# Optimization experiments

Hardware: AMD Instinct MI355X
Metric: run time of the kernel (lower is better)

The kernel has to match this reference:

```python
import jax, jax.numpy as jnp
import numpy as np

V = 25000
E = 100000
NODE_IN = 74
EDGE_IN = 12
OUT = 64
EHID = 128
NUM_STEPS = 6


def setup_inputs() -> dict:
    key = jax.random.key(0)
    ks = jax.random.split(key, 12)
    s = 0.05
    node_feats = jax.random.normal(ks[0], (V, NODE_IN), dtype=jnp.float32)
    edge_feats = jax.random.normal(ks[1], (E, EDGE_IN), dtype=jnp.float32)
    src = jax.random.randint(ks[2], (E,), 0, V)
    dst = jax.random.randint(ks[3], (E,), 0, V)
    # project_node_feats: Linear(node_in, out)
    Wp = jax.random.normal(ks[4], (NODE_IN, OUT), dtype=jnp.float32) * s
    bp = jnp.zeros((OUT,), dtype=jnp.float32)
    # edge network: Linear(edge_in, ehid) -> ReLU -> Linear(ehid, out*out)
    We1 = jax.random.normal(ks[5], (EDGE_IN, EHID), dtype=jnp.float32) * s
    be1 = jnp.zeros((EHID,), dtype=jnp.float32)
    We2 = jax.random.normal(ks[6], (EHID, OUT * OUT), dtype=jnp.float32) * s
    be2 = jnp.zeros((OUT * OUT,), dtype=jnp.float32)
    # NNConv output bias
    bias = jnp.zeros((OUT,), dtype=jnp.float32)
    return {
        "node_feats": node_feats, "edge_feats": edge_feats,
        "src": src, "dst": dst,
        "Wp": Wp, "bp": bp,
        "We1": We1, "be1": be1, "We2": We2, "be2": be2,
        "bias": bias,
    }


def reference(node_feats, edge_feats, src, dst, Wp, bp, We1, be1, We2, be2, bias):
    # project node features
    h = jax.nn.relu(node_feats @ Wp + bp)  # [V, OUT]
    # per-edge weight matrices (same every step -> hoist out of loop)
    ew = jax.nn.relu(edge_feats @ We1 + be1) @ We2 + be2  # [E, OUT*OUT]
    ew = ew.reshape(E, OUT, OUT)
    for _ in range(NUM_STEPS):
        # gather src node feats, batched matvec, scatter-sum to dst
        msg = jnp.einsum('ei,eio->eo', h[src], ew)  # [E, OUT]
        agg = jax.ops.segment_sum(msg, dst, num_segments=V)  # [V, OUT]
        h = jax.nn.relu(agg + bias)
    return h
```

## Files before the change

kernel.cpp:

```cpp
#include <hip/hip_runtime.h>
#include <hip/hip_bf16.h>

#define Vn 25000
#define En 100000
#define NODE_IN 74
#define EDGE_IN 12
#define OUTD 64
#define EHID 128
#define NUM_STEPS 6

typedef __attribute__((ext_vector_type(8))) _Float16 half8;
typedef __attribute__((ext_vector_type(4))) float floatx4;

__global__ void proj_kernel(const float* __restrict__ node,
                            const float* __restrict__ Wp,
                            const float* __restrict__ bp,
                            float* __restrict__ h) {
  __shared__ float nf[NODE_IN];
  int v = blockIdx.x;
  int o = threadIdx.x;
  for (int i = o; i < NODE_IN; i += 64) nf[i] = node[(size_t)v * NODE_IN + i];
  __syncthreads();
  float acc = bp[o];
  for (int i = 0; i < NODE_IN; ++i) acc = fmaf(nf[i], Wp[i * OUTD + o], acc);
  h[(size_t)v * OUTD + o] = fmaxf(acc, 0.0f);
}

__global__ void edge_kernel(const float* __restrict__ ef,
                            const float* __restrict__ We1,
                            const float* __restrict__ be1,
                            _Float16* __restrict__ f) {
  __shared__ float es[EDGE_IN];
  int e = blockIdx.x;
  int k = threadIdx.x;
  if (k < EDGE_IN) es[k] = ef[(size_t)e * EDGE_IN + k];
  __syncthreads();
  float acc = be1[k];
  for (int j = 0; j < EDGE_IN; ++j) acc = fmaf(es[j], We1[j * EHID + k], acc);
  f[(size_t)e * EHID + k] = (_Float16)fmaxf(acc, 0.0f);
}

__global__ void w2r_kernel(const float* __restrict__ We2,
                           _Float16* __restrict__ w2s) {
  int g = blockIdx.x * 256 + threadIdx.x;
  int j = g & 7;
  int quad = (g >> 3) & 3;
  int l15 = (g >> 5) & 15;
  int c = (g >> 9) & 3;
  int step = g >> 11;
  int s = step & 3;
  int i = step >> 2;
  int k = s * 32 + quad * 8 + j;
  int col = i * 64 + c * 16 + l15;
  int eidx = g & 2047;
  int estore = eidx ^ (((eidx >> 6) & 3) << 3);
  w2s[((size_t)step << 11) | estore] = (_Float16)We2[(size_t)k * (OUTD * OUTD) + col];
}

#define GLOAD_LDS(gp, lp)                                                     \
  __builtin_amdgcn_global_load_lds(                                           \
      (const __attribute__((address_space(1))) void*)(gp),                    \
      (__attribute__((address_space(3))) void*)(lp), 16, 0, 0)

__global__ __launch_bounds__(64, 2) void msg_kernel(
    const float* __restrict__ h,
    const _Float16* __restrict__ f,
    const _Float16* __restrict__ w2s,
    const int* __restrict__ src,
    const int* __restrict__ dst,
    const float* __restrict__ be2,
    float* __restrict__ agg) {
  __shared__ __align__(16) char smem_raw[16384];
  __shared__ int s_dst[64];

  _Float16* h16 = (_Float16*)smem_raw;
  char* ring = smem_raw + 8192;

  const int lane = threadIdx.x;
  const int quad = lane >> 4;
  const int l15 = lane & 15;
  const int e0 = blockIdx.x * 64;

  {
    int eg = e0 + lane;
    s_dst[lane] = (eg < En) ? dst[eg] : -1;
    int sv = (eg < En) ? src[eg] : 0;
    const float4* hp = reinterpret_cast<const float4*>(h + (size_t)sv * OUTD);
#pragma unroll
    for (int c = 0; c < 16; ++c) {
      float4 v = hp[c];
      h16[(c * 4 + 0) * 64 + lane] = (_Float16)v.x;
      h16[(c * 4 + 1) * 64 + lane] = (_Float16)v.y;
      h16[(c * 4 + 2) * 64 + lane] = (_Float16)v.z;
      h16[(c * 4 + 3) * 64 + lane] = (_Float16)v.w;
    }
  }

  half8 afr[4][4];
#pragma unroll
  for (int t = 0; t < 4; ++t) {
    int e = e0 + t * 16 + l15;
    if (e >= En) e = En - 1;
    const _Float16* fr = f + (size_t)e * EHID + quad * 8;
#pragma unroll
    for (int s = 0; s < 4; ++s)
      afr[t][s] = *reinterpret_cast<const half8*>(fr + s * 32);
  }

  floatx4 acc[4][4];
  const floatx4 zero4 = (floatx4){0.f, 0.f, 0.f, 0.f};
#pragma unroll
  for (int t = 0; t < 4; ++t)
#pragma unroll
    for (int c = 0; c < 4; ++c) acc[t][c] = zero4;

  const char* w2b = (const char*)w2s;
  const int roff = l15 * 64 + ((quad ^ ((l15 >> 1) & 3)) << 4);
  const char* sp0 = ring + roff;
  const char* sp1 = ring + 4096 + roff;

#define STAGE(GS, SLOT)                                                       \
  {                                                                           \
    const char* gp_ = w2b + (size_t)(GS) * 4096 + lane * 16;                  \
    char* lp_ = ring + (SLOT) * 4096;                                         \
    GLOAD_LDS(gp_, lp_);                                                      \
    GLOAD_LDS(gp_ + 1024, lp_ + 1024);                                        \
    GLOAD_LDS(gp_ + 2048, lp_ + 2048);                                        \
    GLOAD_LDS(gp_ + 3072, lp_ + 3072);                                        \
  }

#define VM4 asm volatile("s_waitcnt vmcnt(4)" ::: "memory")
#define LGKM0 asm volatile("s_waitcnt lgkmcnt(0)" ::: "memory")
#define SB __builtin_amdgcn_sched_barrier(0)

#define KSTEP(SS, BMM, BRD, STSLOT, RDP, GST)                                 \
  {                                                                           \
    LGKM0;                                                                    \
    SB;                                                                       \
    int gs_ = (GST) > 255 ? 255 : (GST);                                      \
    STAGE(gs_, STSLOT);                                                       \
    VM4;                                                                      \
    BRD[0] = *reinterpret_cast<const half8*>(RDP);                            \
    BRD[1] = *reinterpret_cast<const half8*>(RDP + 1024);                     \
    BRD[2] = *reinterpret_cast<const half8*>(RDP + 2048);                     \
    BRD[3] = *reinterpret_cast<const half8*>(RDP + 3072);                     \
    __builtin_amdgcn_s_setprio(1);                                            \
    _Pragma("unroll") for (int t = 0; t < 4; ++t) {                           \
      half8 as = afr[t][SS] * hb[t];                                          \
      acc[t][0] = __builtin_amdgcn_mfma_f32_16x16x32_f16(as, BMM[0], acc[t][0], 0, 0, 0); \
      acc[t][1] = __builtin_amdgcn_mfma_f32_16x16x32_f16(as, BMM[1], acc[t][1], 0, 0, 0); \
      acc[t][2] = __builtin_amdgcn_mfma_f32_16x16x32_f16(as, BMM[2], acc[t][2], 0, 0, 0); \
      acc[t][3] = __builtin_amdgcn_mfma_f32_16x16x32_f16(as, BMM[3], acc[t][3], 0, 0, 0); \
    }                                                                         \
    __builtin_amdgcn_s_setprio(0);                                            \
  }

  STAGE(0, 0);
  STAGE(1, 1);
  VM4;
  half8 P[4], Q[4];
  P[0] = *reinterpret_cast<const half8*>(sp0);
  P[1] = *reinterpret_cast<const half8*>(sp0 + 1024);
  P[2] = *reinterpret_cast<const half8*>(sp0 + 2048);
  P[3] = *reinterpret_cast<const half8*>(sp0 + 3072);

  for (int i = 0; i < 64; ++i) {
    half8 hb[4];
#pragma unroll
    for (int t = 0; t < 4; ++t) {
      _Float16 hf = h16[i * 64 + t * 16 + l15];
      hb[t] = (half8){hf, hf, hf, hf, hf, hf, hf, hf};
    }
    int j = i * 4;
    KSTEP(0, P, Q, 0, sp1, j + 2);
    KSTEP(1, Q, P, 1, sp0, j + 3);
    KSTEP(2, P, Q, 0, sp1, j + 4);
    KSTEP(3, Q, P, 1, sp0, j + 5);
  }

  {
#pragma unroll
    for (int s = 0; s < 2; ++s) {
      half8 b2f[4];
#pragma unroll
      for (int c = 0; c < 4; ++c) {
        half8 v;
#pragma unroll
        for (int j = 0; j < 8; ++j)
          v[j] = (_Float16)be2[(s * 32 + quad * 8 + j) * 64 + c * 16 + l15];
        b2f[c] = v;
      }
#pragma unroll
      for (int t = 0; t < 4; ++t) {
        half8 ha;
#pragma unroll
        for (int j = 0; j < 8; ++j)
          ha[j] = h16[(s * 32 + quad * 8 + j) * 64 + t * 16 + l15];
#pragma unroll
        for (int c = 0; c < 4; ++c)
          acc[t][c] = __builtin_amdgcn_mfma_f32_16x16x32_f16(ha, b2f[c], acc[t][c], 0, 0, 0);
      }
    }
  }

#pragma unroll
  for (int t = 0; t < 4; ++t) {
    int rb = t * 16 + quad * 4;
#pragma unroll
    for (int c = 0; c < 4; ++c) {
      int col = c * 16 + l15;
#pragma unroll
      for (int r = 0; r < 4; ++r) {
        int d = s_dst[rb + r];
        if (d >= 0) atomicAdd(&agg[(size_t)d * OUTD + col], acc[t][c][r]);
      }
    }
  }
}

__global__ void update_kernel(float* __restrict__ agg,
                              const float* __restrict__ bias,
                              float* __restrict__ hout,
                              float* __restrict__ dout, int last) {
  int g = blockIdx.x * 256 + threadIdx.x;
  if (g >= Vn * OUTD) return;
  float v = agg[g];
  agg[g] = 0.0f;
  float r = fmaxf(v + bias[g & 63], 0.0f);
  hout[g] = r;
  if (last) dout[g] = r;
}

extern "C" void kernel_launch(void* const* d_in, const int* in_sizes, int n_in,
                              void* d_out, int out_size, void* d_ws, size_t ws_size,
                              hipStream_t stream) {
  const float* node = (const float*)d_in[0];
  const float* edge = (const float*)d_in[1];
  const int* src = (const int*)d_in[2];
  const int* dst = (const int*)d_in[3];
  const float* Wp   = (const float*)d_in[4];
  const float* bp   = (const float*)d_in[5];
  const float* We1  = (const float*)d_in[6];
  const float* be1  = (const float*)d_in[7];
  const float* We2  = (const float*)d_in[8];
  const float* be2  = (const float*)d_in[9];
  const float* bias = (const float*)d_in[10];
  float* out = (float*)d_out;

  char* ws = (char*)d_ws;
  float* agg = (float*)(ws);
  float* h_a = (float*)(ws + 6400000);
  float* h_b = (float*)(ws + 12800000);
  _Float16* f   = (_Float16*)(ws + 19200000);
  _Float16* w2s = (_Float16*)(ws + 44800000);

  hipMemsetAsync(agg, 0, (size_t)Vn * OUTD * sizeof(float), stream);
  proj_kernel<<<Vn, 64, 0, stream>>>(node, Wp, bp, h_a);
  edge_kernel<<<En, 128, 0, stream>>>(edge, We1, be1, f);
  w2r_kernel<<<(OUTD * OUTD * EHID) / 256, 256, 0, stream>>>(We2, w2s);

  float* hin = h_a;
  float* hout = h_b;
  for (int s = 0; s < NUM_STEPS; ++s) {
    msg_kernel<<<(En + 63) / 64, 64, 0, stream>>>(hin, f, w2s, src, dst, be2, agg);
    update_kernel<<<(Vn * OUTD + 255) / 256, 256, 0, stream>>>(
        agg, bias, hout, out, s == NUM_STEPS - 1);
    float* t = hin; hin = hout; hout = t;
  }
}
```

Baseline: 856.7 us.

## Split message kernel reduction over input dim across two blocks per edge tile

Each 64-edge tile is now processed by two blocks, each covering half of the input dimension (32 of 64 rows of the per-edge weight). Partial results from both halves are combined through the existing atomic adds. The h tile in shared memory is halved and stored with a transposed layout so four values can be read as one half4 vector. Launch bounds go up to four blocks per SM. The aim is more parallelism and occupancy, paid for by doubling atomic traffic, redundantly loading the edge-feature fragments and src/dst, and issuing twice as many blocks.

Result: slower. 2.169 ms (+153.2%).

```diff
diff --git a/kernel.cpp b/kernel.cpp
--- a/kernel.cpp
+++ b/kernel.cpp
@@ -10,6 +10,7 @@
 #define NUM_STEPS 6
 
 typedef __attribute__((ext_vector_type(8))) _Float16 half8;
+typedef __attribute__((ext_vector_type(4))) _Float16 half4;
 typedef __attribute__((ext_vector_type(4))) float floatx4;
 
 __global__ void proj_kernel(const float* __restrict__ node,
@@ -62,7 +63,7 @@
       (const __attribute__((address_space(1))) void*)(gp),                    \
       (__attribute__((address_space(3))) void*)(lp), 16, 0, 0)
 
-__global__ __launch_bounds__(64, 2) void msg_kernel(
+__global__ __launch_bounds__(64, 4) void msg_kernel(
     const float* __restrict__ h,
     const _Float16* __restrict__ f,
     const _Float16* __restrict__ w2s,
@@ -70,29 +71,35 @@
     const int* __restrict__ dst,
     const float* __restrict__ be2,
     float* __restrict__ agg) {
-  __shared__ __align__(16) char smem_raw[16384];
+  __shared__ __align__(16) char smem_raw[12288];
   __shared__ int s_dst[64];
 
   _Float16* h16 = (_Float16*)smem_raw;
-  char* ring = smem_raw + 8192;
+  char* ring = smem_raw + 4096;
 
   const int lane = threadIdx.x;
   const int quad = lane >> 4;
   const int l15 = lane & 15;
-  const int e0 = blockIdx.x * 64;
+  const int tile = blockIdx.x >> 1;
+  const int ihalf = blockIdx.x & 1;
+  const int e0 = tile * 64;
+  const int SBASE = ihalf * 128;
+  const int SMAX = SBASE + 127;
 
   {
     int eg = e0 + lane;
     s_dst[lane] = (eg < En) ? dst[eg] : -1;
     int sv = (eg < En) ? src[eg] : 0;
-    const float4* hp = reinterpret_cast<const float4*>(h + (size_t)sv * OUTD);
-#pragma unroll
-    for (int c = 0; c < 16; ++c) {
+    const float4* hp = reinterpret_cast<const float4*>(h + (size_t)sv * OUTD + ihalf * 32);
+    int pe = (l15 << 2) + quad;
+#pragma unroll
+    for (int c = 0; c < 8; ++c) {
       float4 v = hp[c];
-      h16[(c * 4 + 0) * 64 + lane] = (_Float16)v.x;
-      h16[(c * 4 + 1) * 64 + lane] = (_Float16)v.y;
-      h16[(c * 4 + 2) * 64 + lane] = (_Float16)v.z;
-      h16[(c * 4 + 3) * 64 + lane] = (_Float16)v.w;
+      int li = c * 4;
+      h16[(li + 0) * 64 + pe] = (_Float16)v.x;
+      h16[(li + 1) * 64 + pe] = (_Float16)v.y;
+      h16[(li + 2) * 64 + pe] = (_Float16)v.z;
+      h16[(li + 3) * 64 + pe] = (_Float16)v.w;
     }
   }
 
@@ -137,7 +144,7 @@
   {                                                                           \
     LGKM0;                                                                    \
     SB;                                                                       \
-    int gs_ = (GST) > 255 ? 255 : (GST);                                      \
+    int gs_ = (GST) > SMAX ? SMAX : (GST);                                    \
     STAGE(gs_, STSLOT);                                                       \
     VM4;                                                                      \
     BRD[0] = *reinterpret_cast<const half8*>(RDP);                            \
@@ -155,8 +162,8 @@
     __builtin_amdgcn_s_setprio(0);                                            \
   }
 
-  STAGE(0, 0);
-  STAGE(1, 1);
+  STAGE(SBASE, 0);
+  STAGE(SBASE + 1, 1);
   VM4;
   half8 P[4], Q[4];
   P[0] = *reinterpret_cast<const half8*>(sp0);
@@ -164,42 +171,40 @@
   P[2] = *reinterpret_cast<const half8*>(sp0 + 2048);
   P[3] = *reinterpret_cast<const half8*>(sp0 + 3072);
 
-  for (int i = 0; i < 64; ++i) {
+  for (int li = 0; li < 32; ++li) {
+    half4 hv = *reinterpret_cast<const half4*>(h16 + li * 64 + l15 * 4);
     half8 hb[4];
 #pragma unroll
     for (int t = 0; t < 4; ++t) {
-      _Float16 hf = h16[i * 64 + t * 16 + l15];
+      _Float16 hf = hv[t];
       hb[t] = (half8){hf, hf, hf, hf, hf, hf, hf, hf};
     }
-    int j = i * 4;
-    KSTEP(0, P, Q, 0, sp1, j + 2);
-    KSTEP(1, Q, P, 1, sp0, j + 3);
-    KSTEP(2, P, Q, 0, sp1, j + 4);
-    KSTEP(3, Q, P, 1, sp0, j + 5);
+    int gs = SBASE + li * 4;
+    KSTEP(0, P, Q, 0, sp1, gs + 2);
+    KSTEP(1, Q, P, 1, sp0, gs + 3);
+    KSTEP(2, P, Q, 0, sp1, gs + 4);
+    KSTEP(3, Q, P, 1, sp0, gs + 5);
   }
 
   {
-#pragma unroll
-    for (int s = 0; s < 2; ++s) {
-      half8 b2f[4];
-#pragma unroll
-      for (int c = 0; c < 4; ++c) {
-        half8 v;
-#pragma unroll
-        for (int j = 0; j < 8; ++j)
-          v[j] = (_Float16)be2[(s * 32 + quad * 8 + j) * 64 + c * 16 + l15];
-        b2f[c] = v;
-      }
-#pragma unroll
-      for (int t = 0; t < 4; ++t) {
-        half8 ha;
-#pragma unroll
-        for (int j = 0; j < 8; ++j)
-          ha[j] = h16[(s * 32 + quad * 8 + j) * 64 + t * 16 + l15];
-#pragma unroll
-        for (int c = 0; c < 4; ++c)
-          acc[t][c] = __builtin_amdgcn_mfma_f32_16x16x32_f16(ha, b2f[c], acc[t][c], 0, 0, 0);
-      }
+    half8 b2f[4];
+#pragma unroll
+    for (int c = 0; c < 4; ++c) {
+      half8 v;
+#pragma unroll
+      for (int j = 0; j < 8; ++j)
+        v[j] = (_Float16)be2[(ihalf * 32 + quad * 8 + j) * 64 + c * 16 + l15];
+      b2f[c] = v;
+    }
+#pragma unroll
+    for (int t = 0; t < 4; ++t) {
+      half8 ha;
+#pragma unroll
+      for (int j = 0; j < 8; ++j)
+        ha[j] = h16[(quad * 8 + j) * 64 + l15 * 4 + t];
+#pragma unroll
+      for (int c = 0; c < 4; ++c)
+        acc[t][c] = __builtin_amdgcn_mfma_f32_16x16x32_f16(ha, b2f[c], acc[t][c], 0, 0, 0);
     }
   }
 
@@ -261,8 +266,9 @@
 
   float* hin = h_a;
   float* hout = h_b;
+  const int ntiles = (En + 63) / 64;
   for (int s = 0; s < NUM_STEPS; ++s) {
-    msg_kernel<<<(En + 63) / 64, 64, 0, stream>>>(hin, f, w2s, src, dst, be2, agg);
+    msg_kernel<<<ntiles * 2, 64, 0, stream>>>(hin, f, w2s, src, dst, be2, agg);
     update_kernel<<<(Vn * OUTD + 255) / 256, 256, 0, stream>>>(
         agg, bias, hout, out, s == NUM_STEPS - 1);
     float* t = hin; hin = hout; hout = t;
```

## Share staged edge-weight tiles across four waves per 128-edge block

Applied to the files above, without the earlier changes.

The message kernel now runs 256-thread blocks of four waves, each wave owning 32 edges. All four waves cooperatively stage each 4KB We2 slice into a 4-slot LDS ring, with each wave loading one quarter. This halves the We2 traffic from L2 per edge compared with the old one-wave, 64-edge blocks. The price is a block-wide barrier on every k-step and half as many MFMA tiles per wave to cover latency. The h gather layout is also changed so each lane reads its two edge values with a single half2 load, prefetched one iteration ahead.

Result: faster. 820.6 us (-4.2%).

```diff
diff --git a/kernel.cpp b/kernel.cpp
--- a/kernel.cpp
+++ b/kernel.cpp
@@ -10,6 +10,7 @@
 #define NUM_STEPS 6
 
 typedef __attribute__((ext_vector_type(8))) _Float16 half8;
+typedef __attribute__((ext_vector_type(2))) _Float16 half2v;
 typedef __attribute__((ext_vector_type(4))) float floatx4;
 
 __global__ void proj_kernel(const float* __restrict__ node,
@@ -62,7 +63,7 @@
       (const __attribute__((address_space(1))) void*)(gp),                    \
       (__attribute__((address_space(3))) void*)(lp), 16, 0, 0)
 
-__global__ __launch_bounds__(64, 2) void msg_kernel(
+__global__ __launch_bounds__(256, 3) void msg_kernel(
     const float* __restrict__ h,
     const _Float16* __restrict__ f,
     const _Float16* __restrict__ w2s,
@@ -70,36 +71,46 @@
     const int* __restrict__ dst,
     const float* __restrict__ be2,
     float* __restrict__ agg) {
-  __shared__ __align__(16) char smem_raw[16384];
-  __shared__ int s_dst[64];
-
-  _Float16* h16 = (_Float16*)smem_raw;
-  char* ring = smem_raw + 8192;
-
-  const int lane = threadIdx.x;
+  __shared__ __align__(16) char smem_raw[32768];
+  __shared__ int s_dst[128];
+
+  const int tid = threadIdx.x;
+  const int wv = tid >> 6;
+  const int lane = tid & 63;
   const int quad = lane >> 4;
   const int l15 = lane & 15;
-  const int e0 = blockIdx.x * 64;
-
+  const int e0 = blockIdx.x * 128;
+  const int ew0 = e0 + wv * 32;
+
+  _Float16* h16w = (_Float16*)(smem_raw + wv * 4096);
+  char* ring = smem_raw + 16384;
+
+  if (lane < 32) {
+    int eg = ew0 + lane;
+    s_dst[wv * 32 + lane] = (eg < En) ? dst[eg] : -1;
+  }
   {
-    int eg = e0 + lane;
-    s_dst[lane] = (eg < En) ? dst[eg] : -1;
+    int el = lane & 31;
+    int ih = lane >> 5;
+    int eg = ew0 + el;
     int sv = (eg < En) ? src[eg] : 0;
-    const float4* hp = reinterpret_cast<const float4*>(h + (size_t)sv * OUTD);
-#pragma unroll
-    for (int c = 0; c < 16; ++c) {
+    const float4* hp = reinterpret_cast<const float4*>(h + (size_t)sv * OUTD + ih * 32);
+    int pe = (el & 15) * 2 + (el >> 4);
+#pragma unroll
+    for (int c = 0; c < 8; ++c) {
       float4 v = hp[c];
-      h16[(c * 4 + 0) * 64 + lane] = (_Float16)v.x;
-      h16[(c * 4 + 1) * 64 + lane] = (_Float16)v.y;
-      h16[(c * 4 + 2) * 64 + lane] = (_Float16)v.z;
-      h16[(c * 4 + 3) * 64 + lane] = (_Float16)v.w;
-    }
-  }
-
-  half8 afr[4][4];
-#pragma unroll
-  for (int t = 0; t < 4; ++t) {
-    int e = e0 + t * 16 + l15;
+      int i4 = ih * 32 + c * 4;
+      h16w[(i4 + 0) * 32 + pe] = (_Float16)v.x;
+      h16w[(i4 + 1) * 32 + pe] = (_Float16)v.y;
+      h16w[(i4 + 2) * 32 + pe] = (_Float16)v.z;
+      h16w[(i4 + 3) * 32 + pe] = (_Float16)v.w;
+    }
+  }
+
+  half8 afr[2][4];
+#pragma unroll
+  for (int t = 0; t < 2; ++t) {
+    int e = ew0 + t * 16 + l15;
     if (e >= En) e = En - 1;
     const _Float16* fr = f + (size_t)e * EHID + quad * 8;
 #pragma unroll
@@ -107,10 +118,10 @@
       afr[t][s] = *reinterpret_cast<const half8*>(fr + s * 32);
   }
 
-  floatx4 acc[4][4];
+  floatx4 acc[2][4];
   const floatx4 zero4 = (floatx4){0.f, 0.f, 0.f, 0.f};
 #pragma unroll
-  for (int t = 0; t < 4; ++t)
+  for (int t = 0; t < 2; ++t)
 #pragma unroll
     for (int c = 0; c < 4; ++c) acc[t][c] = zero4;
 
@@ -118,65 +129,66 @@
   const int roff = l15 * 64 + ((quad ^ ((l15 >> 1) & 3)) << 4);
   const char* sp0 = ring + roff;
   const char* sp1 = ring + 4096 + roff;
-
-#define STAGE(GS, SLOT)                                                       \
+  const char* sp2 = ring + 8192 + roff;
+  const char* sp3 = ring + 12288 + roff;
+
+#define STAGE1(GS, SLOT)                                                      \
   {                                                                           \
-    const char* gp_ = w2b + (size_t)(GS) * 4096 + lane * 16;                  \
-    char* lp_ = ring + (SLOT) * 4096;                                         \
+    const char* gp_ = w2b + (size_t)(GS) * 4096 + (wv << 10) + lane * 16;     \
+    char* lp_ = ring + (SLOT) * 4096 + (wv << 10);                            \
     GLOAD_LDS(gp_, lp_);                                                      \
-    GLOAD_LDS(gp_ + 1024, lp_ + 1024);                                        \
-    GLOAD_LDS(gp_ + 2048, lp_ + 2048);                                        \
-    GLOAD_LDS(gp_ + 3072, lp_ + 3072);                                        \
-  }
-
-#define VM4 asm volatile("s_waitcnt vmcnt(4)" ::: "memory")
-#define LGKM0 asm volatile("s_waitcnt lgkmcnt(0)" ::: "memory")
-#define SB __builtin_amdgcn_sched_barrier(0)
-
-#define KSTEP(SS, BMM, BRD, STSLOT, RDP, GST)                                 \
+  }
+
+  asm volatile("s_waitcnt vmcnt(0)" ::: "memory");
+
+  STAGE1(0, 0);
+  STAGE1(1, 1);
+  STAGE1(2, 2);
+
+  half2v hv = *reinterpret_cast<const half2v*>(h16w + l15 * 2);
+  half2v hvn;
+
+#define KSTEP(SS, SPS, GST)                                                   \
   {                                                                           \
-    LGKM0;                                                                    \
-    SB;                                                                       \
+    asm volatile("s_waitcnt vmcnt(2)" ::: "memory");                          \
+    asm volatile("s_barrier" ::: "memory");                                   \
+    half8 B0 = *reinterpret_cast<const half8*>(SPS);                          \
+    half8 B1 = *reinterpret_cast<const half8*>(SPS + 1024);                   \
+    half8 B2 = *reinterpret_cast<const half8*>(SPS + 2048);                   \
+    half8 B3 = *reinterpret_cast<const half8*>(SPS + 3072);                   \
     int gs_ = (GST) > 255 ? 255 : (GST);                                      \
-    STAGE(gs_, STSLOT);                                                       \
-    VM4;                                                                      \
-    BRD[0] = *reinterpret_cast<const half8*>(RDP);                            \
-    BRD[1] = *reinterpret_cast<const half8*>(RDP + 1024);                     \
-    BRD[2] = *reinterpret_cast<const half8*>(RDP + 2048);                     \
-    BRD[3] = *reinterpret_cast<const half8*>(RDP + 3072);                     \
+    STAGE1(gs_, ((SS) + 3) & 3);                                              \
     __builtin_amdgcn_s_setprio(1);                                            \
-    _Pragma("unroll") for (int t = 0; t < 4; ++t) {                           \
+    _Pragma("unroll") for (int t = 0; t < 2; ++t) {                           \
       half8 as = afr[t][SS] * hb[t];                                          \
-      acc[t][0] = __builtin_amdgcn_mfma_f32_16x16x32_f16(as, BMM[0], acc[t][0], 0, 0, 0); \
-      acc[t][1] = __builtin_amdgcn_mfma_f32_16x16x32_f16(as, BMM[1], acc[t][1], 0, 0, 0); \
-      acc[t][2] = __builtin_amdgcn_mfma_f32_16x16x32_f16(as, BMM[2], acc[t][2], 0, 0, 0); \
-      acc[t][3] = __builtin_amdgcn_mfma_f32_16x16x32_f16(as, BMM[3], acc[t][3], 0, 0, 0); \
+      acc[t][0] = __builtin_amdgcn_mfma_f32_16x16x32_f16(as, B0, acc[t][0], 0, 0, 0); \
+      acc[t][1] = __builtin_amdgcn_mfma_f32_16x16x32_f16(as, B1, acc[t][1], 0, 0, 0); \
+      acc[t][2] = __builtin_amdgcn_mfma_f32_16x16x32_f16(as, B2, acc[t][2], 0, 0, 0); \
+      acc[t][3] = __builtin_amdgcn_mfma_f32_16x16x32_f16(as, B3, acc[t][3], 0, 0, 0); \
     }                                                                         \
     __builtin_amdgcn_s_setprio(0);                                            \
   }
 
-  STAGE(0, 0);
-  STAGE(1, 1);
-  VM4;
-  half8 P[4], Q[4];
-  P[0] = *reinterpret_cast<const half8*>(sp0);
-  P[1] = *reinterpret_cast<const half8*>(sp0 + 1024);
-  P[2] = *reinterpret_cast<const half8*>(sp0 + 2048);
-  P[3] = *reinterpret_cast<const half8*>(sp0 + 3072);
-
   for (int i = 0; i < 64; ++i) {
-    half8 hb[4];
-#pragma unroll
-    for (int t = 0; t < 4; ++t) {
-      _Float16 hf = h16[i * 64 + t * 16 + l15];
+    half8 hb[2];
+#pragma unroll
+    for (int t = 0; t < 2; ++t) {
+      _Float16 hf = hv[t];
       hb[t] = (half8){hf, hf, hf, hf, hf, hf, hf, hf};
     }
-    int j = i * 4;
-    KSTEP(0, P, Q, 0, sp1, j + 2);
-    KSTEP(1, Q, P, 1, sp0, j + 3);
-    KSTEP(2, P, Q, 0, sp1, j + 4);
-    KSTEP(3, Q, P, 1, sp0, j + 5);
-  }
+    int gs = i * 4;
+    KSTEP(0, sp0, gs + 3);
+    {
+      int inx = (i < 63) ? i + 1 : 63;
+      hvn = *reinterpret_cast<const half2v*>(h16w + inx * 32 + l15 * 2);
+    }
+    KSTEP(1, sp1, gs + 4);
+    KSTEP(2, sp2, gs + 5);
+    KSTEP(3, sp3, gs + 6);
+    hv = hvn;
+  }
+
+  asm volatile("s_waitcnt vmcnt(0)" ::: "memory");
 
   {
 #pragma unroll
@@ -191,11 +203,11 @@
         b2f[c] = v;
       }
 #pragma unroll
-      for (int t = 0; t < 4; ++t) {
+      for (int t = 0; t < 2; ++t) {
         half8 ha;
 #pragma unroll
         for (int j = 0; j < 8; ++j)
-          ha[j] = h16[(s * 32 + quad * 8 + j) * 64 + t * 16 + l15];
+          ha[j] = h16w[(s * 32 + quad * 8 + j) * 32 + l15 * 2 + t];
 #pragma unroll
         for (int c = 0; c < 4; ++c)
           acc[t][c] = __builtin_amdgcn_mfma_f32_16x16x32_f16(ha, b2f[c], acc[t][c], 0, 0, 0);
@@ -204,8 +216,8 @@
   }
 
 #pragma unroll
-  for (int t = 0; t < 4; ++t) {
-    int rb = t * 16 + quad * 4;
+  for (int t = 0; t < 2; ++t) {
+    int rb = wv * 32 + t * 16 + quad * 4;
 #pragma unroll
     for (int c = 0; c < 4; ++c) {
       int col = c * 16 + l15;
@@ -261,8 +273,9 @@
 
   float* hin = h_a;
   float* hout = h_b;
+  const int nblocks = (En + 127) / 128;
   for (int s = 0; s < NUM_STEPS; ++s) {
-    msg_kernel<<<(En + 63) / 64, 64, 0, stream>>>(hin, f, w2s, src, dst, be2, agg);
+    msg_kernel<<<nblocks, 256, 0, stream>>>(hin, f, w2s, src, dst, be2, agg);
     update_kernel<<<(Vn * OUTD + 255) / 256, 256, 0, stream>>>(
         agg, bias, hout, out, s == NUM_STEPS - 1);
     float* t = hin; hin = hout; hout = t;
```
